# Performance work log

Measured on AMD Instinct MI355X. Metric: run time of the kernel, lower is better.

The kernel has to match this reference:

```python
import jax, jax.numpy as jnp
import numpy as np
import math

D_MODEL = 1024
N_HEADS = 16
D_K = D_MODEL // N_HEADS
R_TYPES = 8
B, S = 2, 2048


def setup_inputs() -> dict:
    key = jax.random.key(0)
    ks = jax.random.split(key, 12)
    sc = 0.02
    return {
        "x": jax.random.normal(ks[0], (B, S, D_MODEL), jnp.float32),
        "Wq": jax.random.normal(ks[1], (D_MODEL, D_MODEL), jnp.float32) * sc,
        "bq": jax.random.normal(ks[2], (D_MODEL,), jnp.float32) * sc,
        "Wk": jax.random.normal(ks[3], (D_MODEL, D_MODEL), jnp.float32) * sc,
        "bk": jax.random.normal(ks[4], (D_MODEL,), jnp.float32) * sc,
        "Wv": jax.random.normal(ks[5], (D_MODEL, D_MODEL), jnp.float32) * sc,
        "bv": jax.random.normal(ks[6], (D_MODEL,), jnp.float32) * sc,
        "Wo": jax.random.normal(ks[7], (D_MODEL, D_MODEL), jnp.float32) * sc,
        "bo": jax.random.normal(ks[8], (D_MODEL,), jnp.float32) * sc,
        "resource_bias": jax.random.normal(ks[9], (N_HEADS, R_TYPES, R_TYPES), jnp.float32),
        "resource_mask": jax.random.randint(ks[10], (B, S), 0, R_TYPES, jnp.int32),
        "attention_mask": jnp.ones((B, S), jnp.int32),
    }


def reference(x, resource_mask, attention_mask, Wq, bq, Wk, bk, Wv, bv, Wo, bo, resource_bias):
    # torch nn.Linear: y = x @ W.T + b
    def lin(h, W, b):
        return jnp.einsum("bsd,ed->bse", h, W) + b

    def split_heads(t):  # [B,S,D] -> [B,H,S,d_k]
        return t.reshape(B, S, N_HEADS, D_K).transpose(0, 2, 1, 3)

    Q = split_heads(lin(x, Wq, bq))
    K = split_heads(lin(x, Wk, bk))
    V = split_heads(lin(x, Wv, bv))

    scores = jnp.einsum("bhid,bhjd->bhij", Q, K) / math.sqrt(D_K)  # [B,H,S,S]

    # vectorized resource-bias gather: bias[h, r_i, r_j] added to scores[b,h,i,j]
    r = resource_mask.astype(jnp.int32)  # values guaranteed < R_TYPES
    # resource_bias[:, r[b,i], r[b,j]] -> [B,H,S,S]
    bias = resource_bias[:, r[:, :, None], r[:, None, :]]  # [H,B,S,S]
    scores = scores + bias.transpose(1, 0, 2, 3)

    mask = attention_mask[:, None, None, :]  # [B,1,1,S] broadcast to [B,H,S,S]
    scores = jnp.where(mask == 0, jnp.float32(-1e9), scores)

    attn = jax.nn.softmax(scores, axis=-1)  # dropout is identity in eval
    out = jnp.einsum("bhij,bhjd->bhid", attn, V)
    out = out.transpose(0, 2, 1, 3).reshape(B, S, D_MODEL)
    return jnp.einsum("bsd,ed->bse", out, Wo) + bo
```

## Files before the change

### kernel.cpp

```cpp
#include <hip/hip_runtime.h>
#include <cstdint>

#define D_MODEL 1024
#define NHEADS  16
#define DKH     64
#define SEQ     2048
#define NBATCH  2
#define MROWS   (NBATCH*SEQ)
#define RTYPES  8
#define LOG2E   1.44269504f

typedef __bf16 bf16;
typedef __bf16 bf16x4v __attribute__((ext_vector_type(4)));
typedef __bf16 bf16x8v __attribute__((ext_vector_type(8)));
typedef float  f32x4v  __attribute__((ext_vector_type(4)));
typedef float  f32x8v  __attribute__((ext_vector_type(8)));
typedef float  f32x16v __attribute__((ext_vector_type(16)));

typedef unsigned int __attribute__((address_space(1))) as1_u32;
typedef unsigned int __attribute__((address_space(3))) as3_u32;

static __device__ __forceinline__ void gload_lds16(const void* g, void* l) {
  __builtin_amdgcn_global_load_lds((const as1_u32*)(uintptr_t)g,
                                   (as3_u32*)(uintptr_t)l, 16, 0, 0);
}

static __device__ __forceinline__ f32x4v mfma16(bf16x8v a, bf16x8v b, f32x4v c) {
  return __builtin_amdgcn_mfma_f32_16x16x32_bf16(a, b, c, 0, 0, 0);
}
static __device__ __forceinline__ f32x16v mfma32(bf16x8v a, bf16x8v b, f32x16v c) {
  return __builtin_amdgcn_mfma_f32_32x32x16_bf16(a, b, c, 0, 0, 0);
}

__global__ void convert_kernel(const float* __restrict__ x,  const float* __restrict__ wq,
                               const float* __restrict__ wk, const float* __restrict__ wv,
                               const float* __restrict__ wo,
                               bf16* __restrict__ xb,  bf16* __restrict__ wqb,
                               bf16* __restrict__ wkb, bf16* __restrict__ wvb,
                               bf16* __restrict__ wob,
                               const float* __restrict__ rbias,
                               const int* __restrict__ rmask,
                               const int* __restrict__ amask,
                               float* __restrict__ biasg)
{
  int idx = blockIdx.x*256 + threadIdx.x;
  if (idx < 1048576){
    float4 v = ((const float4*)x)[idx];
    bf16x4v o = { (bf16)v.x, (bf16)v.y, (bf16)v.z, (bf16)v.w };
    ((bf16x4v*)xb)[idx] = o;
  } else if (idx < 2097152){
    int r = (idx - 1048576) >> 18;
    int i = (idx - 1048576) & 262143;
    const float* src; bf16* dst;
    if (r == 0)      { src = wq; dst = wqb; }
    else if (r == 1) { src = wk; dst = wkb; }
    else if (r == 2) { src = wv; dst = wvb; }
    else             { src = wo; dst = wob; }
    float4 v = ((const float4*)src)[i];
    bf16x4v o = { (bf16)v.x, (bf16)v.y, (bf16)v.z, (bf16)v.w };
    ((bf16x4v*)dst)[i] = o;
  } else {
    int i = idx - 2097152;
    #pragma unroll
    for (int bb=0; bb<NBATCH; bb++){
      int id2 = bb*(NHEADS*RTYPES*SEQ) + i;
      int j  = id2 & (SEQ-1);
      int t  = (id2 >> 11) & 7;
      int hh = (id2 >> 14) & 15;
      int rj = rmask[bb*SEQ + j];
      float am = amask[bb*SEQ + j] ? 0.f : -1e9f;
      biasg[id2] = (rbias[(hh*RTYPES + t)*RTYPES + rj] + am) * LOG2E;
    }
  }
}

struct GemmOuts { const bf16* W[3]; const float* bia[3]; void* out[3]; };

template<int FUSED>
__global__ __launch_bounds__(256, 3) void gemm_bt_kernel(
    const bf16* __restrict__ A, GemmOuts args, float qscale)
{
  const int K  = D_MODEL;
  const int z  = FUSED ? blockIdx.z : 0;
  const bf16*  Bw   = args.W[z];
  const float* bias = args.bia[z];
  void* outp        = args.out[z];
  const float scale = (FUSED && z==0) ? qscale : 1.0f;

  const int n0 = blockIdx.x*128, m0 = blockIdx.y*128;
  const int tid = threadIdx.x;
  const int w = tid>>6, lane = tid&63, g = lane>>4, c = lane&15;
  const int wm = w>>1, wn = w&1;

  __shared__ __align__(16) bf16 a_lds[2][128*32];
  __shared__ __align__(16) bf16 b_lds[2][128*32];

  const f32x4v fzero = {0.f,0.f,0.f,0.f};
  f32x4v acc[4][4];
  for (int i=0;i<4;i++) for (int j=0;j<4;j++) acc[i][j] = fzero;

  const int srow = tid>>2, sc8 = tid&3;

  auto STAGE = [&](int k0, int nb){
    gload_lds16(A  + (size_t)(m0+srow)*K     + k0 + sc8*8, &a_lds[nb][(w*64)*8]);
    gload_lds16(Bw + (size_t)(n0+srow)*K     + k0 + sc8*8, &b_lds[nb][(w*64)*8]);
    gload_lds16(A  + (size_t)(m0+64+srow)*K  + k0 + sc8*8, &a_lds[nb][(256 + w*64)*8]);
    gload_lds16(Bw + (size_t)(n0+64+srow)*K  + k0 + sc8*8, &b_lds[nb][(256 + w*64)*8]);
  };

  auto COMPUTE = [&](int nb){
    bf16x8v af[4], bfv[4];
    #pragma unroll
    for (int mt=0;mt<4;mt++)
      af[mt] = *(const bf16x8v*)&a_lds[nb][(wm*64 + mt*16 + c)*32 + g*8];
    #pragma unroll
    for (int nt=0;nt<4;nt++)
      bfv[nt] = *(const bf16x8v*)&b_lds[nb][(wn*64 + nt*16 + c)*32 + g*8];
    #pragma unroll
    for (int mt=0;mt<4;mt++)
      #pragma unroll
      for (int nt=0;nt<4;nt++)
        acc[mt][nt] = mfma16(af[mt], bfv[nt], acc[mt][nt]);
  };

  STAGE(0, 0);
  __syncthreads();
  int cur = 0;
  for (int k0=32; k0<K; k0+=32){
    STAGE(k0, cur^1);
    COMPUTE(cur);
    __syncthreads();
    cur ^= 1;
  }
  COMPUTE(cur);

  #pragma unroll
  for (int mt=0;mt<4;mt++){
    #pragma unroll
    for (int nt=0;nt<4;nt++){
      if (FUSED && z == 2){
        int m = m0 + wm*64 + mt*16 + g*4;
        int n = n0 + wn*64 + nt*16 + c;
        int bb=m>>11, s=m&2047, hh=n>>6, dk=n&63;
        float bn = bias[n];
        bf16x4v ov;
        #pragma unroll
        for (int r=0;r<4;r++) ov[r] = (bf16)(acc[mt][nt][r] + bn);
        *(bf16x4v*)&((bf16*)outp)[(((size_t)bb*NHEADS+hh)*DKH + dk)*SEQ + s] = ov;
      } else {
        #pragma unroll
        for (int r=0;r<4;r++){
          int m = m0 + wm*64 + mt*16 + g*4 + r;
          int n = n0 + wn*64 + nt*16 + c;
          float v = acc[mt][nt][r] + bias[n];
          if (FUSED){
            v *= scale;
            int bb=m>>11, s=m&2047, hh=n>>6, dk=n&63;
            ((bf16*)outp)[(((size_t)bb*NHEADS+hh)*SEQ + s)*DKH + dk] = (bf16)v;
          } else {
            ((float*)outp)[(size_t)m*D_MODEL + n] = v;
          }
        }
      }
    }
  }
}

__global__ __launch_bounds__(256, 2) void attn5_kernel(
    const bf16* __restrict__ Qg, const bf16* __restrict__ Kg,
    const bf16* __restrict__ Vtg, const float* __restrict__ biasg,
    const int* __restrict__ rmask, bf16* __restrict__ Og)
{
  const int b = blockIdx.z, h = blockIdx.y, q0 = blockIdx.x*128;
  const int tid = threadIdx.x;
  const int w = tid>>6, lane = tid&63;
  const int q5 = lane&31, hi = lane>>5;
  const int bh = b*NHEADS + h;
  const int NT = SEQ/64;

  __shared__ __align__(16) bf16  k_lds[3][64*64];
  __shared__ __align__(16) bf16  vt_lds[3][64*64];
  __shared__ __align__(16) float bias_lds[3][8*64];

  const int qrow = q0 + w*32 + q5;
  const bf16* qptr = Qg + ((size_t)bh*SEQ + qrow)*DKH;
  bf16x8v qf[4];
  #pragma unroll
  for (int kc=0;kc<4;kc++)
    qf[kc] = *(const bf16x8v*)(qptr + kc*16 + hi*8);

  const int tq = rmask[b*SEQ + qrow];

  int boff[2][4];
  #pragma unroll
  for (int nt=0;nt<2;nt++){
    const int j00 = nt*32 + hi*8;
    boff[nt][0] = tq*64 + ((j00 +  0) ^ (tq*8));
    boff[nt][1] = tq*64 + ((j00 +  4) ^ (tq*8));
    boff[nt][2] = tq*64 + ((j00 + 16) ^ (tq*8));
    boff[nt][3] = tq*64 + ((j00 + 20) ^ (tq*8));
  }

  bf16x8v ones;
  #pragma unroll
  for (int i=0;i<8;i++) ones[i] = (bf16)1.0f;

  f32x16v oacc[2];
  #pragma unroll
  for (int dt=0;dt<2;dt++)
    #pragma unroll
    for (int r=0;r<16;r++) oacc[dt][r] = 0.f;
  f32x16v lacc;
  #pragma unroll
  for (int r=0;r<16;r++) lacc[r] = 0.f;
  float mrow = -1e30f;

  auto STAGE = [&](int j0, int nb){
    #pragma unroll
    for (int i=0;i<2;i++){
      const int chunk = i*256 + tid;
      const int p = chunk>>3, c8 = chunk&7;
      const int jsrc = (p & 32) + (p & 3) + (((p>>3)&1)<<2) + (((p>>2)&1)<<3) + (p & 16);
      const int dsrc = (c8 ^ (p&7)) << 3;
      gload_lds16(Kg  + ((size_t)bh*SEQ + j0 + jsrc)*DKH + dsrc, &k_lds[nb][(i*256 + w*64)*8]);
      gload_lds16(Vtg + ((size_t)bh*DKH + p)*SEQ + j0 + dsrc,    &vt_lds[nb][(i*256 + w*64)*8]);
    }
    if (w < 2){
      const int chunk = w*64 + lane;
      const int t = chunk>>4, c16 = chunk&15;
      const int jsw = (c16<<2) ^ (t<<3);
      gload_lds16(biasg + ((size_t)(bh*RTYPES + t))*SEQ + j0 + jsw, &bias_lds[nb][w*256]);
    }
  };

  auto COMPUTE = [&](int nb){
    const char*  kb_ = (const char*)k_lds[nb];
    const char*  vb_ = (const char*)vt_lds[nb];
    const float* bb_ = &bias_lds[nb][0];

    f32x16v s[2];
    #pragma unroll
    for (int nt=0;nt<2;nt++){
      f32x4v b0 = *(const f32x4v*)&bb_[boff[nt][0]];
      f32x4v b1 = *(const f32x4v*)&bb_[boff[nt][1]];
      f32x4v b2 = *(const f32x4v*)&bb_[boff[nt][2]];
      f32x4v b3 = *(const f32x4v*)&bb_[boff[nt][3]];
      f32x8v h0 = __builtin_shufflevector(b0, b1, 0,1,2,3,4,5,6,7);
      f32x8v h1 = __builtin_shufflevector(b2, b3, 0,1,2,3,4,5,6,7);
      s[nt] = __builtin_shufflevector(h0, h1, 0,1,2,3,4,5,6,7,8,9,10,11,12,13,14,15);
      #pragma unroll
      for (int kc=0;kc<4;kc++){
        const int row = nt*32 + q5;
        bf16x8v kf = *(const bf16x8v*)(kb_ + row*128 + ((kc*32 + hi*16) ^ ((row&7)<<4)));
        s[nt] = mfma32(kf, qf[kc], s[nt]);
      }
    }

    float mx = s[0][0];
    #pragma unroll
    for (int r=1;r<16;r++) mx = fmaxf(mx, s[0][r]);
    #pragma unroll
    for (int r=0;r<16;r++) mx = fmaxf(mx, s[1][r]);
    mx = fmaxf(mx, __shfl_xor(mx, 32));

    if (!__all(mx - mrow <= 8.0f)){
      float mnew = fmaxf(mrow, mx);
      float scl = exp2f(mrow - mnew);
      #pragma unroll
      for (int dt=0;dt<2;dt++)
        #pragma unroll
        for (int r=0;r<16;r++) oacc[dt][r] *= scl;
      #pragma unroll
      for (int r=0;r<16;r++) lacc[r] *= scl;
      mrow = mnew;
    }

    #pragma unroll
    for (int nt=0;nt<2;nt++)
      #pragma unroll
      for (int r=0;r<16;r++)
        s[nt][r] = exp2f(s[nt][r] - mrow);

    bf16x8v pa[4];
    #pragma unroll
    for (int m=0;m<4;m++)
      #pragma unroll
      for (int e=0;e<8;e++)
        pa[m][e] = (bf16)s[m>>1][e + (m&1)*8];

    #pragma unroll
    for (int m=0;m<4;m++) lacc = mfma32(ones, pa[m], lacc);

    #pragma unroll
    for (int dt=0;dt<2;dt++){
      #pragma unroll
      for (int m=0;m<4;m++){
        const int row = dt*32 + q5;
        bf16x8v vf = *(const bf16x8v*)(vb_ + row*128 + ((m*32 + hi*16) ^ ((row&7)<<4)));
        oacc[dt] = mfma32(vf, pa[m], oacc[dt]);
      }
    }
  };

  STAGE(0, 0);
  STAGE(64, 1);
  if (w < 2) asm volatile("s_waitcnt vmcnt(5)" ::: "memory");
  else       asm volatile("s_waitcnt vmcnt(4)" ::: "memory");
  __builtin_amdgcn_s_barrier();

  int cur = 0;
  for (int t=0; t<NT; ++t){
    if (t+2 < NT){
      int nb2 = cur+2; if (nb2 >= 3) nb2 -= 3;
      STAGE((t+2)*64, nb2);
    }
    COMPUTE(cur);
    if (t+2 < NT){
      if (w < 2) asm volatile("s_waitcnt vmcnt(5)" ::: "memory");
      else       asm volatile("s_waitcnt vmcnt(4)" ::: "memory");
    } else {
      asm volatile("s_waitcnt vmcnt(0)" ::: "memory");
    }
    __builtin_amdgcn_s_barrier();
    cur = (cur+1 == 3) ? 0 : cur+1;
  }

  const float inv = 1.0f / lacc[0];
  #pragma unroll
  for (int dt=0;dt<2;dt++){
    #pragma unroll
    for (int rq=0;rq<4;rq++){
      bf16x4v ov;
      #pragma unroll
      for (int k=0;k<4;k++) ov[k] = (bf16)(oacc[dt][rq*4+k] * inv);
      const int d = dt*32 + 8*rq + 4*hi;
      *(bf16x4v*)&Og[(size_t)(b*SEQ + qrow)*D_MODEL + h*DKH + d] = ov;
    }
  }
}

extern "C" void kernel_launch(void* const* d_in, const int* in_sizes, int n_in,
                              void* d_out, int out_size, void* d_ws, size_t ws_size,
                              hipStream_t stream)
{
  (void)in_sizes; (void)n_in; (void)out_size; (void)ws_size;
  const float* x     = (const float*)d_in[0];
  const float* Wq    = (const float*)d_in[1];
  const float* bq    = (const float*)d_in[2];
  const float* Wk    = (const float*)d_in[3];
  const float* bk    = (const float*)d_in[4];
  const float* Wv    = (const float*)d_in[5];
  const float* bv    = (const float*)d_in[6];
  const float* Wo    = (const float*)d_in[7];
  const float* bo    = (const float*)d_in[8];
  const float* rbias = (const float*)d_in[9];
  const int*   rmask = (const int*)d_in[10];
  const int*   amask = (const int*)d_in[11];
  float* out = (float*)d_out;

  char* ws = (char*)d_ws;
  bf16*  xb    = (bf16*)(ws);
  bf16*  wqb   = (bf16*)(ws + (8u<<20));
  bf16*  wkb   = (bf16*)(ws + (10u<<20));
  bf16*  wvb   = (bf16*)(ws + (12u<<20));
  bf16*  wob   = (bf16*)(ws + (14u<<20));
  bf16*  qb    = (bf16*)(ws + (16u<<20));
  bf16*  kb    = (bf16*)(ws + (24u<<20));
  bf16*  vtb   = (bf16*)(ws + (32u<<20));
  bf16*  aob   = (bf16*)(ws + (40u<<20));
  float* biasg = (float*)(ws + (48u<<20));

  convert_kernel<<<9216, 256, 0, stream>>>(x,Wq,Wk,Wv,Wo, xb,wqb,wkb,wvb,wob,
                                           rbias, rmask, amask, biasg);

  GemmOuts qkv;
  qkv.W[0]=wqb; qkv.W[1]=wkb; qkv.W[2]=wvb;
  qkv.bia[0]=bq; qkv.bia[1]=bk; qkv.bia[2]=bv;
  qkv.out[0]=qb; qkv.out[1]=kb; qkv.out[2]=vtb;
  gemm_bt_kernel<1><<<dim3(D_MODEL/128, MROWS/128, 3), 256, 0, stream>>>(xb, qkv, 0.125f*LOG2E);

  attn5_kernel<<<dim3(SEQ/128, NHEADS, NBATCH), 256, 0, stream>>>(qb, kb, vtb, biasg, rmask, aob);

  GemmOuts og;
  og.W[0]=wob; og.W[1]=wob; og.W[2]=wob;
  og.bia[0]=bo; og.bia[1]=bo; og.bia[2]=bo;
  og.out[0]=out; og.out[1]=out; og.out[2]=out;
  gemm_bt_kernel<0><<<dim3(D_MODEL/128, MROWS/128), 256, 0, stream>>>(aob, og, 1.0f);
}
```

Measured before the change: 136.9 us.

## Load bias directly from global into registers and use conflict-free unswizzled LDS layout

The attention kernel no longer stages the resource-bias table through LDS. Each lane instead loads its own bias row straight from global memory into registers, one tile ahead of use. The K/V staging now uses a permuted source-row mapping, so each lane's MFMA fragment sits at a plain contiguous LDS offset with no XOR swizzle, which simplifies address computation. The main loop is kept rolled (unroll 1) and the max reduction is rebalanced into a tree. The cost is more per-lane global traffic and exposed latency for bias loads, plus possible LDS bank conflicts without the swizzle.

Result: slower. 156.8 us (+14.5%).

```diff
diff --git a/kernel.cpp b/kernel.cpp
--- a/kernel.cpp
+++ b/kernel.cpp
@@ -14,7 +14,6 @@
 typedef __bf16 bf16x4v __attribute__((ext_vector_type(4)));
 typedef __bf16 bf16x8v __attribute__((ext_vector_type(8)));
 typedef float  f32x4v  __attribute__((ext_vector_type(4)));
-typedef float  f32x8v  __attribute__((ext_vector_type(8)));
 typedef float  f32x16v __attribute__((ext_vector_type(16)));
 
 typedef unsigned int __attribute__((address_space(1))) as1_u32;
@@ -166,7 +165,7 @@
   }
 }
 
-__global__ __launch_bounds__(256, 2) void attn5_kernel(
+__global__ __launch_bounds__(256, 2) void attn6_kernel(
     const bf16* __restrict__ Qg, const bf16* __restrict__ Kg,
     const bf16* __restrict__ Vtg, const float* __restrict__ biasg,
     const int* __restrict__ rmask, bf16* __restrict__ Og)
@@ -178,9 +177,8 @@
   const int bh = b*NHEADS + h;
   const int NT = SEQ/64;
 
-  __shared__ __align__(16) bf16  k_lds[3][64*64];
-  __shared__ __align__(16) bf16  vt_lds[3][64*64];
-  __shared__ __align__(16) float bias_lds[3][8*64];
+  __shared__ __align__(16) bf16 k_lds[3][64*64];
+  __shared__ __align__(16) bf16 vt_lds[3][64*64];
 
   const int qrow = q0 + w*32 + q5;
   const bf16* qptr = Qg + ((size_t)bh*SEQ + qrow)*DKH;
@@ -190,136 +188,128 @@
     qf[kc] = *(const bf16x8v*)(qptr + kc*16 + hi*8);
 
   const int tq = rmask[b*SEQ + qrow];
-
-  int boff[2][4];
-  #pragma unroll
-  for (int nt=0;nt<2;nt++){
-    const int j00 = nt*32 + hi*8;
-    boff[nt][0] = tq*64 + ((j00 +  0) ^ (tq*8));
-    boff[nt][1] = tq*64 + ((j00 +  4) ^ (tq*8));
-    boff[nt][2] = tq*64 + ((j00 + 16) ^ (tq*8));
-    boff[nt][3] = tq*64 + ((j00 + 20) ^ (tq*8));
-  }
+  const float* bptrL = biasg + (size_t)(bh*RTYPES + tq)*SEQ;
+
+  const int sig = (lane & 0x33) | ((lane & 8) >> 1) | ((lane & 4) << 1);
+  const bf16* ksrcL = Kg  + ((size_t)bh*SEQ + sig)*DKH;
+  const bf16* vsrcL = Vtg + ((size_t)bh*DKH + lane)*SEQ;
+
+  const int lbase = hi*512 + q5*8;
 
   bf16x8v ones;
   #pragma unroll
   for (int i=0;i<8;i++) ones[i] = (bf16)1.0f;
 
-  f32x16v oacc[2];
-  #pragma unroll
-  for (int dt=0;dt<2;dt++)
-    #pragma unroll
-    for (int r=0;r<16;r++) oacc[dt][r] = 0.f;
-  f32x16v lacc;
-  #pragma unroll
-  for (int r=0;r<16;r++) lacc[r] = 0.f;
+  f32x16v oacc0, oacc1, lacc;
+  #pragma unroll
+  for (int r=0;r<16;r++){ oacc0[r]=0.f; oacc1[r]=0.f; lacc[r]=0.f; }
   float mrow = -1e30f;
 
   auto STAGE = [&](int j0, int nb){
     #pragma unroll
     for (int i=0;i<2;i++){
-      const int chunk = i*256 + tid;
-      const int p = chunk>>3, c8 = chunk&7;
-      const int jsrc = (p & 32) + (p & 3) + (((p>>3)&1)<<2) + (((p>>2)&1)<<3) + (p & 16);
-      const int dsrc = (c8 ^ (p&7)) << 3;
-      gload_lds16(Kg  + ((size_t)bh*SEQ + j0 + jsrc)*DKH + dsrc, &k_lds[nb][(i*256 + w*64)*8]);
-      gload_lds16(Vtg + ((size_t)bh*DKH + p)*SEQ + j0 + dsrc,    &vt_lds[nb][(i*256 + w*64)*8]);
-    }
-    if (w < 2){
-      const int chunk = w*64 + lane;
-      const int t = chunk>>4, c16 = chunk&15;
-      const int jsw = (c16<<2) ^ (t<<3);
-      gload_lds16(biasg + ((size_t)(bh*RTYPES + t))*SEQ + j0 + jsw, &bias_lds[nb][w*256]);
+      const int dblk = i*4 + w;
+      gload_lds16(ksrcL + (size_t)j0*DKH + dblk*8, &k_lds[nb][(i*256 + w*64)*8]);
+      gload_lds16(vsrcL + j0 + dblk*8,             &vt_lds[nb][(i*256 + w*64)*8]);
     }
   };
 
-  auto COMPUTE = [&](int nb){
-    const char*  kb_ = (const char*)k_lds[nb];
-    const char*  vb_ = (const char*)vt_lds[nb];
-    const float* bb_ = &bias_lds[nb][0];
-
-    f32x16v s[2];
+  f32x4v bv[2][4];
+  auto BIAS_LOAD = [&](int j0){
     #pragma unroll
     for (int nt=0;nt<2;nt++){
-      f32x4v b0 = *(const f32x4v*)&bb_[boff[nt][0]];
-      f32x4v b1 = *(const f32x4v*)&bb_[boff[nt][1]];
-      f32x4v b2 = *(const f32x4v*)&bb_[boff[nt][2]];
-      f32x4v b3 = *(const f32x4v*)&bb_[boff[nt][3]];
-      f32x8v h0 = __builtin_shufflevector(b0, b1, 0,1,2,3,4,5,6,7);
-      f32x8v h1 = __builtin_shufflevector(b2, b3, 0,1,2,3,4,5,6,7);
-      s[nt] = __builtin_shufflevector(h0, h1, 0,1,2,3,4,5,6,7,8,9,10,11,12,13,14,15);
-      #pragma unroll
-      for (int kc=0;kc<4;kc++){
-        const int row = nt*32 + q5;
-        bf16x8v kf = *(const bf16x8v*)(kb_ + row*128 + ((kc*32 + hi*16) ^ ((row&7)<<4)));
-        s[nt] = mfma32(kf, qf[kc], s[nt]);
-      }
-    }
-
-    float mx = s[0][0];
-    #pragma unroll
-    for (int r=1;r<16;r++) mx = fmaxf(mx, s[0][r]);
-    #pragma unroll
-    for (int r=0;r<16;r++) mx = fmaxf(mx, s[1][r]);
-    mx = fmaxf(mx, __shfl_xor(mx, 32));
-
-    if (!__all(mx - mrow <= 8.0f)){
-      float mnew = fmaxf(mrow, mx);
-      float scl = exp2f(mrow - mnew);
-      #pragma unroll
-      for (int dt=0;dt<2;dt++)
-        #pragma unroll
-        for (int r=0;r<16;r++) oacc[dt][r] *= scl;
-      #pragma unroll
-      for (int r=0;r<16;r++) lacc[r] *= scl;
-      mrow = mnew;
-    }
-
-    #pragma unroll
-    for (int nt=0;nt<2;nt++)
-      #pragma unroll
-      for (int r=0;r<16;r++)
-        s[nt][r] = exp2f(s[nt][r] - mrow);
-
-    bf16x8v pa[4];
-    #pragma unroll
-    for (int m=0;m<4;m++)
-      #pragma unroll
-      for (int e=0;e<8;e++)
-        pa[m][e] = (bf16)s[m>>1][e + (m&1)*8];
-
-    #pragma unroll
-    for (int m=0;m<4;m++) lacc = mfma32(ones, pa[m], lacc);
-
-    #pragma unroll
-    for (int dt=0;dt<2;dt++){
-      #pragma unroll
-      for (int m=0;m<4;m++){
-        const int row = dt*32 + q5;
-        bf16x8v vf = *(const bf16x8v*)(vb_ + row*128 + ((m*32 + hi*16) ^ ((row&7)<<4)));
-        oacc[dt] = mfma32(vf, pa[m], oacc[dt]);
-      }
+      const float* bpn = bptrL + j0 + nt*32 + hi*8;
+      bv[nt][0] = *(const f32x4v*)(bpn + 0);
+      bv[nt][1] = *(const f32x4v*)(bpn + 4);
+      bv[nt][2] = *(const f32x4v*)(bpn + 16);
+      bv[nt][3] = *(const f32x4v*)(bpn + 20);
     }
   };
 
   STAGE(0, 0);
+  BIAS_LOAD(0);
   STAGE(64, 1);
-  if (w < 2) asm volatile("s_waitcnt vmcnt(5)" ::: "memory");
-  else       asm volatile("s_waitcnt vmcnt(4)" ::: "memory");
+  asm volatile("s_waitcnt vmcnt(4)" ::: "memory");
   __builtin_amdgcn_s_barrier();
 
   int cur = 0;
+  #pragma unroll 1
   for (int t=0; t<NT; ++t){
     if (t+2 < NT){
       int nb2 = cur+2; if (nb2 >= 3) nb2 -= 3;
       STAGE((t+2)*64, nb2);
     }
-    COMPUTE(cur);
-    if (t+2 < NT){
-      if (w < 2) asm volatile("s_waitcnt vmcnt(5)" ::: "memory");
-      else       asm volatile("s_waitcnt vmcnt(4)" ::: "memory");
-    } else {
-      asm volatile("s_waitcnt vmcnt(0)" ::: "memory");
+    {
+      const bf16* kb_ = &k_lds[cur][0];
+      const bf16* vb_ = &vt_lds[cur][0];
+
+      f32x16v s0, s1;
+      #pragma unroll
+      for (int g4=0; g4<4; g4++)
+        #pragma unroll
+        for (int rr=0; rr<4; rr++){
+          s0[g4*4+rr] = bv[0][g4][rr];
+          s1[g4*4+rr] = bv[1][g4][rr];
+        }
+      BIAS_LOAD((t+1 < NT) ? (t+1)*64 : t*64);
+
+      #pragma unroll
+      for (int kc=0;kc<4;kc++){
+        bf16x8v kf0 = *(const bf16x8v*)(kb_ + lbase + kc*1024);
+        bf16x8v kf1 = *(const bf16x8v*)(kb_ + lbase + kc*1024 + 256);
+        s0 = mfma32(kf0, qf[kc], s0);
+        s1 = mfma32(kf1, qf[kc], s1);
+      }
+
+      float a0 = fmaxf(fmaxf(s0[0],s0[1]),s0[2]);
+      float a1 = fmaxf(fmaxf(s0[3],s0[4]),s0[5]);
+      float a2 = fmaxf(fmaxf(s0[6],s0[7]),s0[8]);
+      float a3 = fmaxf(fmaxf(s0[9],s0[10]),s0[11]);
+      float a4 = fmaxf(fmaxf(s0[12],s0[13]),s0[14]);
+      float a5 = fmaxf(fmaxf(s0[15],s1[0]),s1[1]);
+      float a6 = fmaxf(fmaxf(s1[2],s1[3]),s1[4]);
+      float a7 = fmaxf(fmaxf(s1[5],s1[6]),s1[7]);
+      float a8 = fmaxf(fmaxf(s1[8],s1[9]),s1[10]);
+      float a9 = fmaxf(fmaxf(s1[11],s1[12]),s1[13]);
+      float aA = fmaxf(s1[14],s1[15]);
+      float b0 = fmaxf(fmaxf(a0,a1),a2);
+      float b1 = fmaxf(fmaxf(a3,a4),a5);
+      float b2 = fmaxf(fmaxf(a6,a7),a8);
+      float b3 = fmaxf(a9,aA);
+      float mx = fmaxf(fmaxf(b0,b1), fmaxf(b2,b3));
+      mx = fmaxf(mx, __shfl_xor(mx, 32));
+
+      if (!__all(mx - mrow <= 8.0f)){
+        float mnew = fmaxf(mrow, mx);
+        float scl = exp2f(mrow - mnew);
+        #pragma unroll
+        for (int r=0;r<16;r++){ oacc0[r] *= scl; oacc1[r] *= scl; lacc[r] *= scl; }
+        mrow = mnew;
+      }
+
+      #pragma unroll
+      for (int r=0;r<16;r++){ s0[r] = exp2f(s0[r] - mrow); s1[r] = exp2f(s1[r] - mrow); }
+
+      bf16x8v pa0, pa1, pa2, pa3;
+      #pragma unroll
+      for (int e=0;e<8;e++){
+        pa0[e] = (bf16)s0[e];   pa1[e] = (bf16)s0[e+8];
+        pa2[e] = (bf16)s1[e];   pa3[e] = (bf16)s1[e+8];
+      }
+
+      lacc = mfma32(ones, pa0, lacc);
+      lacc = mfma32(ones, pa1, lacc);
+      lacc = mfma32(ones, pa2, lacc);
+      lacc = mfma32(ones, pa3, lacc);
+
+      #pragma unroll
+      for (int m=0;m<4;m++){
+        bf16x8v vf0 = *(const bf16x8v*)(vb_ + lbase + m*1024);
+        bf16x8v vf1 = *(const bf16x8v*)(vb_ + lbase + m*1024 + 256);
+        bf16x8v pm = (m==0)?pa0:(m==1)?pa1:(m==2)?pa2:pa3;
+        oacc0 = mfma32(vf0, pm, oacc0);
+        oacc1 = mfma32(vf1, pm, oacc1);
+      }
     }
     __builtin_amdgcn_s_barrier();
     cur = (cur+1 == 3) ? 0 : cur+1;
@@ -327,15 +317,15 @@
 
   const float inv = 1.0f / lacc[0];
   #pragma unroll
-  for (int dt=0;dt<2;dt++){
-    #pragma unroll
-    for (int rq=0;rq<4;rq++){
-      bf16x4v ov;
-      #pragma unroll
-      for (int k=0;k<4;k++) ov[k] = (bf16)(oacc[dt][rq*4+k] * inv);
-      const int d = dt*32 + 8*rq + 4*hi;
-      *(bf16x4v*)&Og[(size_t)(b*SEQ + qrow)*D_MODEL + h*DKH + d] = ov;
-    }
+  for (int rq=0;rq<4;rq++){
+    bf16x4v ov0, ov1;
+    #pragma unroll
+    for (int k=0;k<4;k++){ ov0[k] = (bf16)(oacc0[rq*4+k] * inv);
+                           ov1[k] = (bf16)(oacc1[rq*4+k] * inv); }
+    const int d = 8*rq + 4*hi;
+    bf16* orow = &Og[(size_t)(b*SEQ + qrow)*D_MODEL + h*DKH];
+    *(bf16x4v*)(orow + d)      = ov0;
+    *(bf16x4v*)(orow + 32 + d) = ov1;
   }
 }
 
@@ -379,7 +369,7 @@
   qkv.out[0]=qb; qkv.out[1]=kb; qkv.out[2]=vtb;
   gemm_bt_kernel<1><<<dim3(D_MODEL/128, MROWS/128, 3), 256, 0, stream>>>(xb, qkv, 0.125f*LOG2E);
 
-  attn5_kernel<<<dim3(SEQ/128, NHEADS, NBATCH), 256, 0, stream>>>(qb, kb, vtb, biasg, rmask, aob);
+  attn6_kernel<<<dim3(SEQ/128, NHEADS, NBATCH), 256, 0, stream>>>(qb, kb, vtb, biasg, rmask, aob);
 
   GemmOuts og;
   og.W[0]=wob; og.W[1]=wob; og.W[2]=wob;
```
